# Kernel tuning notes

Hardware: AMD Instinct MI355X
Metric: run time of the kernel (lower is better)

## Reference

```python
import jax, jax.numpy as jnp
import numpy as np

B, D_K, D_V = 1024, 64, 64
N_FEAT, RANK, K = 32768, 1, 32

def _normalize(a):
    return a / jnp.linalg.norm(a, axis=-1, keepdims=True)

def setup_inputs() -> dict:
    key = jax.random.key(0)
    k0, k1, k2, k3, k4 = jax.random.split(key, 5)
    x = jax.random.normal(k0, (B, D_K, D_V), dtype=jnp.float32)
    V_enc = _normalize(jax.random.normal(k1, (N_FEAT, RANK, D_K), dtype=jnp.float32))
    W_enc = _normalize(jax.random.normal(k2, (N_FEAT, RANK, D_V), dtype=jnp.float32))
    V_dec = _normalize(jax.random.normal(k3, (N_FEAT, RANK, D_K), dtype=jnp.float32))
    W_dec = _normalize(jax.random.normal(k4, (N_FEAT, RANK, D_V), dtype=jnp.float32))
    b_enc = jnp.zeros((N_FEAT,), dtype=jnp.float32)
    bias = jnp.zeros((D_K, D_V), dtype=jnp.float32)
    return {"x": x, "V_enc": V_enc, "W_enc": W_enc, "b_enc": b_enc,
            "V_dec": V_dec, "W_dec": W_dec, "bias": bias}

def reference(x, V_enc, W_enc, b_enc, V_dec, W_dec, bias):
    b, d_k, d_v = x.shape
    n_feat = V_enc.shape[0]
    x_flat = x.reshape(b, d_k * d_v)
    # encode: einsum('irk,bkv,irv->bi') == x_flat @ (sum_r v_ir (x) w_ir)^T
    M_enc = jnp.einsum('irk,irv->ikv', V_enc, W_enc).reshape(n_feat, d_k * d_v)
    pre = x_flat @ M_enc.T + b_enc                       # [B, n_feat]
    # topk activation with relu on the kept values, zeros elsewhere
    vals, idx = jax.lax.top_k(pre, K)                    # [B, K]
    vals = jnp.maximum(vals, 0.0)
    coeffs = jnp.zeros_like(pre).at[jnp.arange(b)[:, None], idx].set(vals)
    # decode: einsum('bi,irk,irv->bkv')
    M_dec = jnp.einsum('irk,irv->ikv', V_dec, W_dec).reshape(n_feat, d_k * d_v)
    recon_flat = coeffs @ M_dec + bias.reshape(-1)
    recon = recon_flat.reshape(b, d_k, d_v)
    mse = jnp.mean((recon_flat - x_flat) ** 2)
    # fresh steps_since_active buffer (zeros) + dead_threshold=100 -> no dead
    # features, so aux_loss == 0 exactly; total loss == mse.
    return recon, coeffs, mse
```

## Files before the change

### kernel.cpp

```cpp
#include <hip/hip_runtime.h>
#include <hip/hip_bf16.h>
#include <hip/hip_fp8.h>
#include <stdint.h>

#define NFEAT 32768
#define BATCH 1024
#define DK 64
#define DV 64
#define DD 4096
#define KSEL 32
#define CAND_CAP 512
#define THRESH 2.70f

using bf16 = __bf16;
using f32x4 = __attribute__((ext_vector_type(4))) float;
using f32x16 = __attribute__((ext_vector_type(16))) float;
using i32x4 = __attribute__((ext_vector_type(4))) int;
using i32x8 = __attribute__((ext_vector_type(8))) int;

__device__ __forceinline__ void gload_lds16(const void* g, void* l) {
  __builtin_amdgcn_global_load_lds((const __attribute__((address_space(1))) void*)g,
                                   (__attribute__((address_space(3))) void*)l,
                                   16, 0, 0);
}


__global__ void k_convert_x(const float* __restrict__ x, unsigned char* __restrict__ xb) {
  int t = threadIdx.x;
  int rb = blockIdx.x >> 3;
  int kg0 = (blockIdx.x & 7) * 16;
  int row = (t & 127) >> 2;
  int cin = ((t >> 7) << 4) + ((t & 3) << 2);
  const float* xrow = x + ((size_t)rb * 32 + row) * DD;
  for (int kg = kg0; kg < kg0 + 16; ++kg) {
    float4 v = *reinterpret_cast<const float4*>(xrow + kg * 32 + cin);
    union { unsigned char b[4]; unsigned u; } o;
    o.b[0] = __hip_fp8_e4m3(v.x).__x;
    o.b[1] = __hip_fp8_e4m3(v.y).__x;
    o.b[2] = __hip_fp8_e4m3(v.z).__x;
    o.b[3] = __hip_fp8_e4m3(v.w).__x;
    *reinterpret_cast<unsigned*>(xb + (((size_t)rb * 128 + kg) << 10) + t * 4) = o.u;
  }
}

__global__ void k_build_menc(const float* __restrict__ Venc, const float* __restrict__ Wenc,
                             unsigned char* __restrict__ Menc) {
  int t = threadIdx.x;
  int rb = blockIdx.x;
  int row = (t & 127) >> 2;
  int cin = ((t >> 7) << 4) + ((t & 3) << 2);
  size_t rowg = (size_t)rb * 32 + row;
  const float* vrow = Venc + rowg * DK;
  float4 w0 = *reinterpret_cast<const float4*>(Wenc + rowg * DV + cin);
  float4 w1 = *reinterpret_cast<const float4*>(Wenc + rowg * DV + 32 + cin);
  unsigned char* base = Menc + ((size_t)rb << 17);
#pragma unroll 4
  for (int kg = 0; kg < 128; ++kg) {
    float vk = 16.0f * vrow[kg >> 1];
    float4 w = (kg & 1) ? w1 : w0;
    union { unsigned char b[4]; unsigned u; } o;
    o.b[0] = __hip_fp8_e4m3(vk * w.x).__x;
    o.b[1] = __hip_fp8_e4m3(vk * w.y).__x;
    o.b[2] = __hip_fp8_e4m3(vk * w.z).__x;
    o.b[3] = __hip_fp8_e4m3(vk * w.w).__x;
    *reinterpret_cast<unsigned*>(base + (kg << 10) + t * 4) = o.u;
  }
}

#define BM 256
#define BN 256
#define BKB 128
#define NT (DD / BKB)
#define ABUF 32768
#define BUFSZ 65536
#define GEMM_LDS (2 * BUFSZ)

__device__ __forceinline__ void stage_chunk(const unsigned char* __restrict__ G, size_t r32base,
                                            int kg0, int c, int lane, char* dstbase) {
  const unsigned char* src = G + (((r32base + (c >> 2)) * 128 + kg0 + (c & 3)) << 10) + lane * 16;
  gload_lds16(src, dstbase + c * 1024);
}

__device__ __forceinline__ i32x8 frag_ld8(const char* base, int chunk, int lane) {
  const char* p = base + chunk * 1024 + (lane & 31) * 16;
  i32x4 lo = *reinterpret_cast<const i32x4*>(p);
  i32x4 hi = *reinterpret_cast<const i32x4*>(p + 512);
  i32x8 r;
  r[0] = lo[0]; r[1] = lo[1]; r[2] = lo[2]; r[3] = lo[3];
  r[4] = hi[0]; r[5] = hi[1]; r[6] = hi[2]; r[7] = hi[3];
  return r;
}

__device__ __forceinline__ int chA(int half, int idx) {
  int g = idx >> 2, kg = idx & 3;
  int mb32 = (g & 1) + ((g >> 1) << 2) + half * 2;
  return mb32 * 4 + kg;
}
__device__ __forceinline__ int chB(int half, int idx) {
  int nb32 = ((idx >> 2) << 1) + half;
  return nb32 * 4 + (idx & 3);
}

#define LD_A(H)                                                                     \
  _Pragma("unroll") for (int mb = 0; mb < 2; ++mb)                                  \
  _Pragma("unroll") for (int kh = 0; kh < 2; ++kh)                                  \
    afr[mb][kh] = frag_ld8(cur, (wr * 4 + (H) * 2 + mb) * 4 + kh * 2 + (lane >> 5), lane);

#define LD_B(H)                                                                     \
  _Pragma("unroll") for (int kh = 0; kh < 2; ++kh)                                  \
    bfr[(H)][kh] = frag_ld8(cur + ABUF, (wc * 2 + (H)) * 4 + kh * 2 + (lane >> 5), lane);

#define ST_A(HALF, KT)                                                              \
  stage_chunk(A, ar32, (KT) * 4, chA(HALF, wave * 2), lane, nxt);                   \
  stage_chunk(A, ar32, (KT) * 4, chA(HALF, wave * 2 + 1), lane, nxt);

#define ST_B(HALF, KT)                                                              \
  stage_chunk(Bt, br32, (KT) * 4, chB(HALF, wave * 2), lane, nxt + ABUF);           \
  stage_chunk(Bt, br32, (KT) * 4, chB(HALF, wave * 2 + 1), lane, nxt + ABUF);

#define MFMA_Q(MH, NB)                                                              \
  asm volatile("s_waitcnt lgkmcnt(0)" ::: "memory");                                \
  __builtin_amdgcn_sched_barrier(0);                                                \
  __builtin_amdgcn_s_setprio(1);                                                    \
  _Pragma("unroll") for (int mb = 0; mb < 2; ++mb)                                  \
  _Pragma("unroll") for (int kh = 0; kh < 2; ++kh)                                  \
    acc[(MH) * 2 + mb][NB] = __builtin_amdgcn_mfma_scale_f32_32x32x64_f8f6f4(       \
        afr[mb][kh], bfr[NB][kh], acc[(MH) * 2 + mb][NB], 0, 0, 0, 0x7F, 0, 0x7F);  \
  __builtin_amdgcn_s_setprio(0);

#define VMC(N) asm volatile("s_waitcnt vmcnt(" #N ")" ::: "memory");
#define LGKM0 asm volatile("s_waitcnt lgkmcnt(0)" ::: "memory");
#define BARR                                                                        \
  asm volatile("s_barrier" ::: "memory");                                           \
  __builtin_amdgcn_sched_barrier(0);

__global__ __launch_bounds__(512, 2)
void k_gemm(const unsigned char* __restrict__ A, const unsigned char* __restrict__ Bt,
            const float* __restrict__ benc, float* __restrict__ coeffs,
            int* __restrict__ cand_idx, int* __restrict__ cand_cnt) {
  extern __shared__ char lds[];
  int tid = threadIdx.x;
  int wave = tid >> 6;
  int lane = tid & 63;
  int wr = wave >> 2;
  int wc = wave & 3;

  int d = blockIdx.x;
  int lw = (d & 7) * 64 + (d >> 3);
  int q = lw >> 2;
  int p = lw & 3;
  size_t brow = (size_t)p * BM;
  size_t bcol = (size_t)q * BN;
  size_t ar32 = brow >> 5;
  size_t br32 = bcol >> 5;

  f32x16 acc[4][2] = {};
  i32x8 afr[2][2];
  i32x8 bfr[2][2];

  {
    char* nxt = lds;
    ST_B(0, 0) ST_A(0, 0) ST_B(1, 0) ST_A(1, 0)
  }
  VMC(2)
  BARR

#pragma unroll 1
  for (int u = 0; u < NT - 1; ++u) {
    char* cur = lds + (u & 1) * BUFSZ;
    char* nxt = lds + ((u + 1) & 1) * BUFSZ;
    int k1 = u + 1;
    LD_A(0) LD_B(0) LD_B(1)
    ST_B(0, k1) ST_A(0, k1) ST_B(1, k1)
    VMC(6)
    BARR
    MFMA_Q(0, 0)
    MFMA_Q(0, 1)
    LD_A(1)
    ST_A(1, k1)
    VMC(2)
    LGKM0
    BARR
    MFMA_Q(1, 1)
    MFMA_Q(1, 0)
  }

  {
    char* cur = lds + ((NT - 1) & 1) * BUFSZ;
    LD_A(0) LD_B(0) LD_B(1)
    VMC(0)
    BARR
    MFMA_Q(0, 0)
    MFMA_Q(0, 1)
    LD_A(1)
    LGKM0
    BARR
    MFMA_Q(1, 1)
    MFMA_Q(1, 0)
  }

  {
    float4 z = {0.f, 0.f, 0.f, 0.f};
#pragma unroll
    for (int it = 0; it < 32; ++it) {
      size_t row = brow + it * 8 + wave;
      *reinterpret_cast<float4*>(coeffs + row * NFEAT + bcol + lane * 4) = z;
    }
  }

#pragma unroll
  for (int nb = 0; nb < 2; ++nb) {
    int col = (int)bcol + wc * 64 + nb * 32 + (lane & 31);
    float be = benc[col];
#pragma unroll
    for (int MB = 0; MB < 4; ++MB) {
      int row0 = (int)brow + wr * 128 + MB * 32 + ((lane >> 5) << 2);
#pragma unroll
      for (int reg = 0; reg < 16; ++reg) {
        int row = row0 + (reg & 3) + ((reg >> 2) << 3);
        float val = acc[MB][nb][reg] * 0.0625f + be;
        if (val > THRESH) {
          int pos = atomicAdd(&cand_cnt[row], 1);
          if (pos < CAND_CAP) cand_idx[row * CAND_CAP + pos] = col;
        }
      }
    }
  }
}

__global__ __launch_bounds__(256, 2)
void k_refine(const float* __restrict__ x,
              const float* __restrict__ Venc,
              const float* __restrict__ Wenc,
              const float* __restrict__ benc,
              const float* __restrict__ Vdec,
              const float* __restrict__ Wdec,
              const float* __restrict__ bias,
              const int* __restrict__ cand_idx,
              const int* __restrict__ cand_cnt,
              float* __restrict__ recon,
              float* __restrict__ coeffs,
              float* __restrict__ msepart) {
  __shared__ float rval[CAND_CAP];
  __shared__ int ridx[CAND_CAP];
  __shared__ float selv[KSEL];
  __shared__ int seli[KSEL];
  __shared__ float Vd[KSEL][DK];
  __shared__ float Wd[KSEL][DV];
  __shared__ float red[256];

  int b = blockIdx.x;
  int t = threadIdx.x;
  int wave = t >> 6;
  int lane = t & 63;

  const float* xr = x + (size_t)b * DD;

  int c = cand_cnt[b];
  if (c > CAND_CAP) c = CAND_CAP;
  for (int i = t; i < c; i += 256) ridx[i] = cand_idx[b * CAND_CAP + i];
  __syncthreads();

  float xreg[DK];
#pragma unroll
  for (int kk = 0; kk < DK; ++kk)
    xreg[kk] = xr[kk * DV + lane];

#pragma unroll 2
  for (int j = wave; j < c; j += 4) {
    int fi = __builtin_amdgcn_readfirstlane(ridx[j]);
    const float* vr = Venc + (size_t)fi * DK;
    float w = Wenc[(size_t)fi * DV + lane];
    float a0 = 0.f, a1 = 0.f, a2 = 0.f, a3 = 0.f;
#pragma unroll
    for (int kk = 0; kk < DK; kk += 4) {
      a0 = fmaf(xreg[kk + 0], vr[kk + 0], a0);
      a1 = fmaf(xreg[kk + 1], vr[kk + 1], a1);
      a2 = fmaf(xreg[kk + 2], vr[kk + 2], a2);
      a3 = fmaf(xreg[kk + 3], vr[kk + 3], a3);
    }
    float p2 = ((a0 + a1) + (a2 + a3)) * w;
#pragma unroll
    for (int off = 1; off < 64; off <<= 1) p2 += __shfl_xor(p2, off);
    if (lane == 0) rval[j] = p2 + benc[fi];
  }
  __syncthreads();

  for (int t2 = t; t2 < c; t2 += 256) {
    float v = rval[t2];
    int fi = ridx[t2];
    int rank = 0;
    for (int j = 0; j < c; ++j) {
      float vj = rval[j];
      if (vj > v || (vj == v && ridx[j] < fi)) ++rank;
    }
    if (rank < KSEL) { selv[rank] = v; seli[rank] = fi; }
  }
  __syncthreads();

  if (t < KSEL) {
    float v = fmaxf(selv[t], 0.f);
    selv[t] = v;
    coeffs[(size_t)b * NFEAT + seli[t]] = v;
  }
  __syncthreads();

  for (int i = t; i < KSEL * DK; i += 256) {
    int s2 = i >> 6, e = i & 63;
    Vd[s2][e] = Vdec[(size_t)seli[s2] * DK + e];
    Wd[s2][e] = Wdec[(size_t)seli[s2] * DV + e];
  }
  __syncthreads();

  int k = t >> 2;
  int vb = (t & 3) << 4;
  float4 r4[4];
#pragma unroll
  for (int g = 0; g < 4; ++g)
    r4[g] = *reinterpret_cast<const float4*>(bias + k * DV + vb + g * 4);
#pragma unroll
  for (int s2 = 0; s2 < KSEL; ++s2) {
    float a = selv[s2] * Vd[s2][k];
    const float4* wrow = reinterpret_cast<const float4*>(&Wd[s2][vb]);
#pragma unroll
    for (int g = 0; g < 4; ++g) {
      float4 wv = wrow[g];
      r4[g].x = fmaf(a, wv.x, r4[g].x);
      r4[g].y = fmaf(a, wv.y, r4[g].y);
      r4[g].z = fmaf(a, wv.z, r4[g].z);
      r4[g].w = fmaf(a, wv.w, r4[g].w);
    }
  }
  float m = 0.f;
  float* ro = recon + (size_t)b * DD + k * DV + vb;
#pragma unroll
  for (int g = 0; g < 4; ++g) {
    float4 xv = *reinterpret_cast<const float4*>(xr + k * DV + vb + g * 4);
    float dx = r4[g].x - xv.x, dy = r4[g].y - xv.y;
    float dz = r4[g].z - xv.z, dw = r4[g].w - xv.w;
    m = fmaf(dx, dx, m); m = fmaf(dy, dy, m);
    m = fmaf(dz, dz, m); m = fmaf(dw, dw, m);
    *reinterpret_cast<float4*>(ro + g * 4) = r4[g];
  }
  red[t] = m;
  __syncthreads();
  for (int s2 = 128; s2 > 0; s2 >>= 1) {
    if (t < s2) red[t] += red[t + s2];
    __syncthreads();
  }
  if (t == 0) msepart[b] = red[0];
}

__global__ void k_mse(const float* __restrict__ msepart, float* __restrict__ out) {
  __shared__ float red[256];
  int t = threadIdx.x;
  float s = 0.f;
  for (int i = t; i < BATCH; i += 256) s += msepart[i];
  red[t] = s;
  __syncthreads();
  for (int k = 128; k > 0; k >>= 1) {
    if (t < k) red[t] += red[t + k];
    __syncthreads();
  }
  if (t == 0) out[0] = red[0] / (float)((size_t)BATCH * DD);
}

extern "C" void kernel_launch(void* const* d_in, const int* in_sizes, int n_in,
                              void* d_out, int out_size, void* d_ws, size_t ws_size,
                              hipStream_t stream) {
  const float* x    = (const float*)d_in[0];
  const float* Venc = (const float*)d_in[1];
  const float* Wenc = (const float*)d_in[2];
  const float* benc = (const float*)d_in[3];
  const float* Vdec = (const float*)d_in[4];
  const float* Wdec = (const float*)d_in[5];
  const float* bias = (const float*)d_in[6];

  float* out = (float*)d_out;
  float* recon  = out;
  float* coeffs = out + (size_t)BATCH * DD;
  float* mse    = coeffs + (size_t)BATCH * NFEAT;

  char* wsp = (char*)d_ws;
  unsigned char* xb8 = (unsigned char*)wsp;   wsp += (size_t)BATCH * DD;
  unsigned char* Menc8 = (unsigned char*)wsp; wsp += (size_t)NFEAT * DD;
  int* cand_idx = (int*)wsp;                  wsp += (size_t)BATCH * CAND_CAP * sizeof(int);
  int* cand_cnt = (int*)wsp;                  wsp += (size_t)BATCH * sizeof(int);
  float* msepart = (float*)wsp;               wsp += (size_t)BATCH * sizeof(float);

  hipFuncSetAttribute((const void*)k_gemm, hipFuncAttributeMaxDynamicSharedMemorySize,
                      GEMM_LDS);

  hipMemsetAsync(cand_cnt, 0, BATCH * sizeof(int), stream);
  k_convert_x<<<256, 256, 0, stream>>>(x, xb8);
  k_build_menc<<<NFEAT / 32, 256, 0, stream>>>(Venc, Wenc, Menc8);
  k_gemm<<<(BATCH / BM) * (NFEAT / BN), 512, GEMM_LDS, stream>>>(xb8, Menc8, benc,
                                                                 coeffs, cand_idx, cand_cnt);
  k_refine<<<BATCH, 256, 0, stream>>>(x, Venc, Wenc, benc, Vdec, Wdec, bias,
                                      cand_idx, cand_cnt, recon, coeffs, msepart);
  k_mse<<<1, 256, 0, stream>>>(msepart, mse);
}
```

Measured before the change: 276.8 us.

## Move coeffs zeroing to memset and stage x in LDS for refine

Drops the zero-fill of the 128 MB coeffs output from the GEMM epilogue and replaces it with a hipMemsetAsync issued before the pipeline. In the refine kernel, x is staged into padded shared memory so each lane reads one row of x with float4 loads. The loop order is swapped so the dot is taken against W_enc, which is a wave-uniform scalar load, and V_enc is then read per lane. This frees the 64 x registers per thread, which lets launch bounds rise to 4 blocks per SM. The memset is a separate full-bandwidth pass that no longer overlaps with GEMM compute.

```diff
diff --git a/kernel.cpp b/kernel.cpp
--- a/kernel.cpp
+++ b/kernel.cpp
@@ -136,7 +136,7 @@
 
 __global__ __launch_bounds__(512, 2)
 void k_gemm(const unsigned char* __restrict__ A, const unsigned char* __restrict__ Bt,
-            const float* __restrict__ benc, float* __restrict__ coeffs,
+            const float* __restrict__ benc,
             int* __restrict__ cand_idx, int* __restrict__ cand_cnt) {
   extern __shared__ char lds[];
   int tid = threadIdx.x;
@@ -199,15 +199,6 @@
     MFMA_Q(1, 0)
   }
 
-  {
-    float4 z = {0.f, 0.f, 0.f, 0.f};
-#pragma unroll
-    for (int it = 0; it < 32; ++it) {
-      size_t row = brow + it * 8 + wave;
-      *reinterpret_cast<float4*>(coeffs + row * NFEAT + bcol + lane * 4) = z;
-    }
-  }
-
 #pragma unroll
   for (int nb = 0; nb < 2; ++nb) {
     int col = (int)bcol + wc * 64 + nb * 32 + (lane & 31);
@@ -228,7 +219,9 @@
   }
 }
 
-__global__ __launch_bounds__(256, 2)
+#define XPAD 68
+
+__global__ __launch_bounds__(256, 4)
 void k_refine(const float* __restrict__ x,
               const float* __restrict__ Venc,
               const float* __restrict__ Wenc,
@@ -241,6 +234,7 @@
               float* __restrict__ recon,
               float* __restrict__ coeffs,
               float* __restrict__ msepart) {
+  __shared__ __align__(16) float xl[DK * XPAD];
   __shared__ float rval[CAND_CAP];
   __shared__ int ridx[CAND_CAP];
   __shared__ float selv[KSEL];
@@ -256,30 +250,32 @@
 
   const float* xr = x + (size_t)b * DD;
 
+  for (int i = (t << 2); i < DD; i += 1024) {
+    float4 v = *reinterpret_cast<const float4*>(xr + i);
+    int k = i >> 6, vv = i & 63;
+    *reinterpret_cast<float4*>(&xl[k * XPAD + vv]) = v;
+  }
+
   int c = cand_cnt[b];
   if (c > CAND_CAP) c = CAND_CAP;
   for (int i = t; i < c; i += 256) ridx[i] = cand_idx[b * CAND_CAP + i];
   __syncthreads();
 
-  float xreg[DK];
-#pragma unroll
-  for (int kk = 0; kk < DK; ++kk)
-    xreg[kk] = xr[kk * DV + lane];
-
-#pragma unroll 2
+  const float* xrow = &xl[lane * XPAD];
   for (int j = wave; j < c; j += 4) {
     int fi = __builtin_amdgcn_readfirstlane(ridx[j]);
-    const float* vr = Venc + (size_t)fi * DK;
-    float w = Wenc[(size_t)fi * DV + lane];
+    const float* wr = Wenc + (size_t)fi * DV;
     float a0 = 0.f, a1 = 0.f, a2 = 0.f, a3 = 0.f;
 #pragma unroll
-    for (int kk = 0; kk < DK; kk += 4) {
-      a0 = fmaf(xreg[kk + 0], vr[kk + 0], a0);
-      a1 = fmaf(xreg[kk + 1], vr[kk + 1], a1);
-      a2 = fmaf(xreg[kk + 2], vr[kk + 2], a2);
-      a3 = fmaf(xreg[kk + 3], vr[kk + 3], a3);
+    for (int v4 = 0; v4 < 16; ++v4) {
+      float4 xv = *reinterpret_cast<const float4*>(xrow + v4 * 4);
+      a0 = fmaf(xv.x, wr[v4 * 4 + 0], a0);
+      a1 = fmaf(xv.y, wr[v4 * 4 + 1], a1);
+      a2 = fmaf(xv.z, wr[v4 * 4 + 2], a2);
+      a3 = fmaf(xv.w, wr[v4 * 4 + 3], a3);
     }
-    float p2 = ((a0 + a1) + (a2 + a3)) * w;
+    float vl = Venc[(size_t)fi * DK + lane];
+    float p2 = ((a0 + a1) + (a2 + a3)) * vl;
 #pragma unroll
     for (int off = 1; off < 64; off <<= 1) p2 += __shfl_xor(p2, off);
     if (lane == 0) rval[j] = p2 + benc[fi];
@@ -392,10 +388,11 @@
                       GEMM_LDS);
 
   hipMemsetAsync(cand_cnt, 0, BATCH * sizeof(int), stream);
+  hipMemsetAsync(coeffs, 0, (size_t)BATCH * NFEAT * sizeof(float), stream);
   k_convert_x<<<256, 256, 0, stream>>>(x, xb8);
   k_build_menc<<<NFEAT / 32, 256, 0, stream>>>(Venc, Wenc, Menc8);
   k_gemm<<<(BATCH / BM) * (NFEAT / BN), 512, GEMM_LDS, stream>>>(xb8, Menc8, benc,
-                                                                 coeffs, cand_idx, cand_cnt);
+                                                                 cand_idx, cand_cnt);
   k_refine<<<BATCH, 256, 0, stream>>>(x, Venc, Wenc, benc, Vdec, Wdec, bias,
                                       cand_idx, cand_cnt, recon, coeffs, msepart);
   k_mse<<<1, 256, 0, stream>>>(msepart, mse);
```

After: 297.4 us. 1.07x slower.
